# Performance work log

Measured on AMD Instinct MI355X. Metric: run time of the kernel, lower is better.

## Reference

```python
import jax, jax.numpy as jnp
import numpy as np

HEAD_NUM = 16
HIDDEN = 1024
HEAD_DIM = HIDDEN // HEAD_NUM


def setup_inputs() -> dict:
    key = jax.random.key(0)
    ks = jax.random.split(key, 9)
    B, S, D = 1, 4096, HIDDEN
    scale = 1.0 / np.sqrt(D)
    inp = {
        "x": jax.random.normal(ks[0], (B, S, D), jnp.float32),
        "wq": jax.random.normal(ks[1], (D, D), jnp.float32) * scale,
        "bq": jnp.zeros((D,), jnp.float32),
        "wk": jax.random.normal(ks[2], (D, D), jnp.float32) * scale,
        "bk": jnp.zeros((D,), jnp.float32),
        "wv": jax.random.normal(ks[3], (D, D), jnp.float32) * scale,
        "bv": jnp.zeros((D,), jnp.float32),
        "wo": jax.random.normal(ks[4], (D, D), jnp.float32) * scale,
        "bo": jnp.zeros((D,), jnp.float32),
    }
    return inp


def reference(x, wq, bq, wk, bk, wv, bv, wo, bo):
    B, S, D = x.shape
    H, Hd = HEAD_NUM, HEAD_DIM
    # QKV projections (weights stored as [in, out])
    q = (x @ wq + bq).reshape(B, S, H, Hd).transpose(0, 2, 1, 3)  # [B,H,S,Hd]
    k = (x @ wk + bk).reshape(B, S, H, Hd).transpose(0, 2, 1, 3)
    v = (x @ wv + bv).reshape(B, S, H, Hd).transpose(0, 2, 1, 3)
    scores = jnp.einsum("bhqd,bhkd->bhqk", q, k) / jnp.sqrt(jnp.float32(Hd))
    attn = jax.nn.softmax(scores, axis=-1)  # dropout in eval mode = identity
    out = jnp.einsum("bhqk,bhkd->bhqd", attn, v)
    out = out.transpose(0, 2, 1, 3).reshape(B, S, D)
    return out @ wo + bo
```

## Files before the change

### kernel.cpp

```cpp
#include <hip/hip_runtime.h>

#define S_LEN  4096
#define DMODEL 1024
#define NHEAD  16
#define HDIM   64

#define QSCALE 0.18033688011112042f

typedef unsigned short u16;
typedef unsigned int   u32;
typedef __bf16 bf16x8 __attribute__((ext_vector_type(8)));
typedef float  f32x4  __attribute__((ext_vector_type(4)));

static __device__ __forceinline__ u16 f2b(float f) {
    union { __bf16 b; u16 u; } c; c.b = (__bf16)f; return c.u;
}

static __device__ __forceinline__ float fexp2(float x) {
#if __has_builtin(__builtin_amdgcn_exp2f)
    return __builtin_amdgcn_exp2f(x);
#else
    return __expf(x * 0.6931471805599453f);
#endif
}

typedef __attribute__((address_space(3))) u32 lds_u32_t;
typedef __attribute__((address_space(1))) const u32 glb_u32_t;
static __device__ __forceinline__ void gload_lds16(const u16* g, u16* l) {
    __builtin_amdgcn_global_load_lds((glb_u32_t*)g, (lds_u32_t*)l, 16, 0, 0);
}

__global__ __launch_bounds__(256)
void convert_x(const float* __restrict__ x, u16* __restrict__ xb) {
    const int i0 = (blockIdx.x * 256 + threadIdx.x) * 8;
    float4 a = *reinterpret_cast<const float4*>(x + i0);
    float4 b = *reinterpret_cast<const float4*>(x + i0 + 4);
    u16 o[8] = {f2b(a.x), f2b(a.y), f2b(a.z), f2b(a.w),
                f2b(b.x), f2b(b.y), f2b(b.z), f2b(b.w)};
    *reinterpret_cast<uint4*>(xb + i0) = *reinterpret_cast<uint4*>(o);
}

__global__ __launch_bounds__(256)
void transpose_w4(const float* __restrict__ w0, const float* __restrict__ w1,
                  const float* __restrict__ w2, const float* __restrict__ w3,
                  u16* __restrict__ wT) {
    const int z = blockIdx.z;
    const float* w = (z == 0) ? w0 : (z == 1) ? w1 : (z == 2) ? w2 : w3;
    u16* dst0 = wT + (size_t)z * DMODEL * DMODEL;
    const int k0 = blockIdx.x * 64, n0 = blockIdx.y * 64;
    const int t = threadIdx.x;
    __shared__ u16 T[64][72];
    const int kk = t >> 4, nn = (t & 15) * 4;
    #pragma unroll
    for (int i = 0; i < 4; ++i) {
        float4 v = *reinterpret_cast<const float4*>(w + (size_t)(k0 + kk + i * 16) * DMODEL + n0 + nn);
        T[nn + 0][kk + i * 16] = f2b(v.x);
        T[nn + 1][kk + i * 16] = f2b(v.y);
        T[nn + 2][kk + i * 16] = f2b(v.z);
        T[nn + 3][kk + i * 16] = f2b(v.w);
    }
    __syncthreads();
    const int n = t >> 2, kc = (t & 3) * 16;
    uint4 r0 = *reinterpret_cast<const uint4*>(&T[n][kc]);
    uint4 r1 = *reinterpret_cast<const uint4*>(&T[n][kc + 8]);
    u16* dst = dst0 + (size_t)(n0 + n) * DMODEL + k0 + kc;
    *reinterpret_cast<uint4*>(dst)     = r0;
    *reinterpret_cast<uint4*>(dst + 8) = r1;
}

template<int MODE>
__global__ __launch_bounds__(256, 2)
void gemm128(const u16* __restrict__ A, const u16* __restrict__ BT,
             const float* __restrict__ b0, const float* __restrict__ b1,
             const float* __restrict__ b2, void* __restrict__ Cout) {
    const int m0 = blockIdx.x * 128;
    const int ny = blockIdx.y;
    const int tz = (MODE == 0) ? (ny >> 3) : 0;
    const int n0 = (MODE == 0) ? ((ny & 7) * 128) : (ny * 128);
    const int tid = threadIdx.x, lane = tid & 63, w = tid >> 6;
    const int wr = w >> 1, wc = w & 1;
    const int fm = lane & 15, fq = lane >> 4;

    __shared__ u16 As[128][32];
    __shared__ u16 Bs[128][32];

    const u16* Bb = BT + (size_t)tz * DMODEL * DMODEL;

    f32x4 acc[4][4];
    #pragma unroll
    for (int i = 0; i < 4; ++i)
        #pragma unroll
        for (int t = 0; t < 4; ++t) acc[i][t] = f32x4{0.f, 0.f, 0.f, 0.f};

    const int srow = lane >> 2, scol = (lane & 3) * 8;

    for (int k0 = 0; k0 < DMODEL; k0 += 32) {
        #pragma unroll
        for (int r = 0; r < 2; ++r) {
            const int rowA = w * 32 + r * 16;
            gload_lds16(A  + (size_t)(m0 + rowA + srow) * DMODEL + k0 + scol, &As[rowA][0]);
            gload_lds16(Bb + (size_t)(n0 + rowA + srow) * DMODEL + k0 + scol, &Bs[rowA][0]);
        }
        __syncthreads();
        bf16x8 af[4], bf[4];
        #pragma unroll
        for (int i = 0; i < 4; ++i) af[i] = *reinterpret_cast<const bf16x8*>(&As[wr * 64 + i * 16 + fm][fq * 8]);
        #pragma unroll
        for (int t = 0; t < 4; ++t) bf[t] = *reinterpret_cast<const bf16x8*>(&Bs[wc * 64 + t * 16 + fm][fq * 8]);
        #pragma unroll
        for (int i = 0; i < 4; ++i)
            #pragma unroll
            for (int t = 0; t < 4; ++t)
                acc[i][t] = __builtin_amdgcn_mfma_f32_16x16x32_bf16(af[i], bf[t], acc[i][t], 0, 0, 0);
        __syncthreads();
    }

    const float* bp = (MODE == 0) ? ((tz == 0) ? b0 : (tz == 1) ? b1 : b2) : b0;
    const float scl = (MODE == 0 && tz == 0) ? QSCALE : 1.0f;
    #pragma unroll
    for (int t = 0; t < 4; ++t) {
        const int col = n0 + wc * 64 + t * 16 + fm;
        const float bias = bp[col];
        if (MODE == 0 && tz == 2) {
            const int hh = col >> 6, d = col & 63;
            u16* vb = (u16*)Cout + (size_t)2 * S_LEN * DMODEL +
                      ((size_t)hh * HDIM + d) * S_LEN;
            #pragma unroll
            for (int i = 0; i < 4; ++i) {
                const int row0 = m0 + wr * 64 + i * 16 + fq * 4;
                u16 o[4] = {f2b(acc[i][t][0] + bias), f2b(acc[i][t][1] + bias),
                            f2b(acc[i][t][2] + bias), f2b(acc[i][t][3] + bias)};
                *reinterpret_cast<uint2*>(vb + row0) = *reinterpret_cast<uint2*>(o);
            }
        } else {
            #pragma unroll
            for (int i = 0; i < 4; ++i) {
                #pragma unroll
                for (int r = 0; r < 4; ++r) {
                    const int row = m0 + wr * 64 + i * 16 + fq * 4 + r;
                    const float v = (acc[i][t][r] + bias) * scl;
                    if (MODE == 0) {
                        const int hh = col >> 6, d = col & 63;
                        ((u16*)Cout)[(size_t)tz * S_LEN * DMODEL +
                                     ((size_t)hh * S_LEN + row) * HDIM + d] = f2b(v);
                    } else {
                        ((float*)Cout)[(size_t)row * DMODEL + col] = v;
                    }
                }
            }
        }
    }
}

__global__ __launch_bounds__(256, 2)
void gemm_o(const u16* __restrict__ A, const u16* __restrict__ BT,
            const float* __restrict__ bias, float* __restrict__ C) {
    const int m0 = blockIdx.x * 128;
    const int n0 = blockIdx.y * 64;
    const int tid = threadIdx.x, lane = tid & 63, w = tid >> 6;
    const int fm = lane & 15, fq = lane >> 4;

    __shared__ u16 As[128][32];
    __shared__ u16 Bs[64][32];

    f32x4 acc[2][4];
    #pragma unroll
    for (int i = 0; i < 2; ++i)
        #pragma unroll
        for (int t = 0; t < 4; ++t) acc[i][t] = f32x4{0.f, 0.f, 0.f, 0.f};

    const int srow = lane >> 2, scol = (lane & 3) * 8;

    for (int k0 = 0; k0 < DMODEL; k0 += 32) {
        #pragma unroll
        for (int r = 0; r < 2; ++r) {
            const int rowA = w * 32 + r * 16;
            gload_lds16(A + (size_t)(m0 + rowA + srow) * DMODEL + k0 + scol, &As[rowA][0]);
        }
        gload_lds16(BT + (size_t)(n0 + w * 16 + srow) * DMODEL + k0 + scol, &Bs[w * 16][0]);
        __syncthreads();
        bf16x8 af[2], bf[4];
        #pragma unroll
        for (int i = 0; i < 2; ++i) af[i] = *reinterpret_cast<const bf16x8*>(&As[w * 32 + i * 16 + fm][fq * 8]);
        #pragma unroll
        for (int t = 0; t < 4; ++t) bf[t] = *reinterpret_cast<const bf16x8*>(&Bs[t * 16 + fm][fq * 8]);
        #pragma unroll
        for (int i = 0; i < 2; ++i)
            #pragma unroll
            for (int t = 0; t < 4; ++t)
                acc[i][t] = __builtin_amdgcn_mfma_f32_16x16x32_bf16(af[i], bf[t], acc[i][t], 0, 0, 0);
        __syncthreads();
    }

    #pragma unroll
    for (int t = 0; t < 4; ++t) {
        const int col = n0 + t * 16 + fm;
        const float b = bias[col];
        #pragma unroll
        for (int i = 0; i < 2; ++i) {
            #pragma unroll
            for (int r = 0; r < 4; ++r) {
                const int row = m0 + w * 32 + i * 16 + fq * 4 + r;
                C[(size_t)row * DMODEL + col] = acc[i][t][r] + b;
            }
        }
    }
}

template<int NSPLIT>
__global__ __launch_bounds__(256, 4)
void attn_kernel(const u16* __restrict__ Q, const u16* __restrict__ K,
                 const u16* __restrict__ V, void* __restrict__ Optr,
                 float* __restrict__ Lp) {
    const int qt = blockIdx.x, h = blockIdx.y;
    const int sp = (NSPLIT > 1) ? blockIdx.z : 0;
    const int tid = threadIdx.x, lane = tid & 63, wid = tid >> 6;
    const int fm = lane & 15, fq = lane >> 4;

    __shared__ alignas(16) u16 Pt[128][36];
    __shared__ alignas(16) u16 Ks[64][68];
    __shared__ alignas(16) u16 Vt[64][68];

    const u16* Qh = Q + (size_t)h * S_LEN * HDIM;
    const u16* Kh = K + (size_t)h * S_LEN * HDIM;
    const u16* Vh = V + (size_t)h * S_LEN * HDIM;

    const int srow = tid >> 2, sch = (tid & 3) * 16;

    bf16x8 qf[2][2];
    #pragma unroll
    for (int rb = 0; rb < 2; ++rb) {
        const u16* qsrc = Qh + (size_t)(qt * 128 + wid * 32 + rb * 16 + fm) * HDIM + fq * 8;
        qf[rb][0] = *reinterpret_cast<const bf16x8*>(qsrc);
        qf[rb][1] = *reinterpret_cast<const bf16x8*>(qsrc + 32);
    }

    float rsum[2] = {0.f, 0.f};
    f32x4 oacc[2][4];
    #pragma unroll
    for (int rb = 0; rb < 2; ++rb)
        #pragma unroll
        for (int t = 0; t < 4; ++t) oacc[rb][t] = f32x4{0.f, 0.f, 0.f, 0.f};

    const int TOT  = S_LEN / 64;
    const int base = TOT / NSPLIT;
    const int rem  = TOT - base * NSPLIT;
    const int kt0  = sp * base + (sp < rem ? sp : rem);
    const int NT   = base + (sp < rem ? 1 : 0);

    uint4 kr0, kr1, vr0, vr1;
    {
        const u16* ks = Kh + (size_t)(kt0 * 64 + srow) * HDIM + sch;
        kr0 = *reinterpret_cast<const uint4*>(ks);
        kr1 = *reinterpret_cast<const uint4*>(ks + 8);
        const u16* vs = Vh + (size_t)srow * S_LEN + kt0 * 64 + sch;
        vr0 = *reinterpret_cast<const uint4*>(vs);
        vr1 = *reinterpret_cast<const uint4*>(vs + 8);
    }

    for (int it = 0; it < NT; ++it) {
        const int kt = kt0 + it;
        __syncthreads();
        *reinterpret_cast<uint4*>(&Ks[srow][sch])     = kr0;
        *reinterpret_cast<uint4*>(&Ks[srow][sch + 8]) = kr1;
        *reinterpret_cast<uint4*>(&Vt[srow][sch])     = vr0;
        *reinterpret_cast<uint4*>(&Vt[srow][sch + 8]) = vr1;
        __syncthreads();

        if (it + 1 < NT) {
            const u16* ks = Kh + (size_t)((kt + 1) * 64 + srow) * HDIM + sch;
            kr0 = *reinterpret_cast<const uint4*>(ks);
            kr1 = *reinterpret_cast<const uint4*>(ks + 8);
            const u16* vs = Vh + (size_t)srow * S_LEN + (kt + 1) * 64 + sch;
            vr0 = *reinterpret_cast<const uint4*>(vs);
            vr1 = *reinterpret_cast<const uint4*>(vs + 8);
        }

        f32x4 sacc[2][4];
        #pragma unroll
        for (int rb = 0; rb < 2; ++rb)
            #pragma unroll
            for (int mt = 0; mt < 4; ++mt) sacc[rb][mt] = f32x4{0.f, 0.f, 0.f, 0.f};
        __builtin_amdgcn_s_setprio(1);
        #pragma unroll
        for (int kk2 = 0; kk2 < 2; ++kk2) {
            #pragma unroll
            for (int mt = 0; mt < 4; ++mt) {
                bf16x8 kf = *reinterpret_cast<const bf16x8*>(&Ks[mt * 16 + fm][kk2 * 32 + fq * 8]);
                #pragma unroll
                for (int rb = 0; rb < 2; ++rb)
                    sacc[rb][mt] = __builtin_amdgcn_mfma_f32_16x16x32_bf16(kf, qf[rb][kk2], sacc[rb][mt], 0, 0, 0);
            }
        }
        __builtin_amdgcn_s_setprio(0);

        #pragma unroll
        for (int ph = 0; ph < 2; ++ph) {
            #pragma unroll
            for (int rb = 0; rb < 2; ++rb) {
                #pragma unroll
                for (int m2 = 0; m2 < 2; ++m2) {
                    const int mt = ph * 2 + m2;
                    u32 pk[2];
                    float e0 = fexp2(sacc[rb][mt][0]);
                    float e1 = fexp2(sacc[rb][mt][1]);
                    float e2 = fexp2(sacc[rb][mt][2]);
                    float e3 = fexp2(sacc[rb][mt][3]);
                    rsum[rb] += (e0 + e1) + (e2 + e3);
                    pk[0] = (u32)f2b(e0) | ((u32)f2b(e1) << 16);
                    pk[1] = (u32)f2b(e2) | ((u32)f2b(e3) << 16);
                    *reinterpret_cast<uint2*>(&Pt[wid * 32 + rb * 16 + fm][m2 * 16 + fq * 4]) =
                        uint2{pk[0], pk[1]};
                }
            }
            bf16x8 af[2];
            #pragma unroll
            for (int rb = 0; rb < 2; ++rb)
                af[rb] = *reinterpret_cast<const bf16x8*>(&Pt[wid * 32 + rb * 16 + fm][fq * 8]);
            __builtin_amdgcn_s_setprio(1);
            #pragma unroll
            for (int t = 0; t < 4; ++t) {
                bf16x8 bf = *reinterpret_cast<const bf16x8*>(&Vt[t * 16 + fm][ph * 32 + fq * 8]);
                #pragma unroll
                for (int rb = 0; rb < 2; ++rb)
                    oacc[rb][t] = __builtin_amdgcn_mfma_f32_16x16x32_bf16(af[rb], bf, oacc[rb][t], 0, 0, 0);
            }
            __builtin_amdgcn_s_setprio(0);
        }
    }

    if (NSPLIT > 1) {
        float* Op = (float*)Optr + (size_t)sp * S_LEN * DMODEL;
        #pragma unroll
        for (int rb = 0; rb < 2; ++rb) {
            float rs = rsum[rb];
            rs += __shfl_xor(rs, 16, 64);
            rs += __shfl_xor(rs, 32, 64);
            if (fq == 0)
                Lp[(size_t)sp * NHEAD * S_LEN + (size_t)h * S_LEN +
                   qt * 128 + wid * 32 + rb * 16 + fm] = rs;
            #pragma unroll
            for (int t = 0; t < 4; ++t) {
                const int d = t * 16 + fm;
                #pragma unroll
                for (int r = 0; r < 4; ++r) {
                    const int row = qt * 128 + wid * 32 + rb * 16 + fq * 4 + r;
                    Op[(size_t)row * DMODEL + h * HDIM + d] = oacc[rb][t][r];
                }
            }
        }
    } else {
        float l[2][4];
        #pragma unroll
        for (int rb = 0; rb < 2; ++rb) {
            float rs = rsum[rb];
            rs += __shfl_xor(rs, 16, 64);
            rs += __shfl_xor(rs, 32, 64);
            #pragma unroll
            for (int r = 0; r < 4; ++r) l[rb][r] = __shfl(rs, fq * 4 + r, 64);
        }
        u16* O = (u16*)Optr;
        #pragma unroll
        for (int rb = 0; rb < 2; ++rb)
            #pragma unroll
            for (int t = 0; t < 4; ++t) {
                const int d = t * 16 + fm;
                #pragma unroll
                for (int r = 0; r < 4; ++r) {
                    const int row = qt * 128 + wid * 32 + rb * 16 + fq * 4 + r;
                    O[(size_t)row * DMODEL + h * HDIM + d] = f2b(oacc[rb][t][r] / l[rb][r]);
                }
            }
    }
}

template<int NS>
__global__ __launch_bounds__(256)
void combine_o(const float* __restrict__ Op, const float* __restrict__ Lp,
               u16* __restrict__ Ob) {
    const size_t i = ((size_t)blockIdx.x * 256 + threadIdx.x) * 4;
    const int row = (int)(i >> 10), col = (int)(i & 1023);
    const int h = col >> 6;
    float ax = 0.f, ay = 0.f, az = 0.f, aw = 0.f, l = 0.f;
    #pragma unroll
    for (int s = 0; s < NS; ++s) {
        float4 v = *reinterpret_cast<const float4*>(Op + (size_t)s * S_LEN * DMODEL + i);
        ax += v.x; ay += v.y; az += v.z; aw += v.w;
        l += Lp[(size_t)s * NHEAD * S_LEN + (size_t)h * S_LEN + row];
    }
    const float inv = 1.0f / l;
    u16 o[4] = {f2b(ax * inv), f2b(ay * inv), f2b(az * inv), f2b(aw * inv)};
    *reinterpret_cast<uint2*>(Ob + i) = *reinterpret_cast<uint2*>(o);
}

extern "C" void kernel_launch(void* const* d_in, const int* in_sizes, int n_in,
                              void* d_out, int out_size, void* d_ws, size_t ws_size,
                              hipStream_t stream) {
    const float* x  = (const float*)d_in[0];
    const float* wq = (const float*)d_in[1];
    const float* bq = (const float*)d_in[2];
    const float* wk = (const float*)d_in[3];
    const float* bk = (const float*)d_in[4];
    const float* wv = (const float*)d_in[5];
    const float* bv = (const float*)d_in[6];
    const float* wo = (const float*)d_in[7];
    const float* bo = (const float*)d_in[8];

    u16* ws = (u16*)d_ws;
    const size_t MW  = (size_t)DMODEL * DMODEL;
    const size_t NX  = (size_t)S_LEN * DMODEL;
    const size_t TSZ = (size_t)NHEAD * S_LEN * HDIM;

    u16* xb = ws;
    u16* WT = xb + NX;
    u16* Qb = WT + 4 * MW;
    u16* Ob = Qb + 3 * TSZ;
    float* Op = (float*)(Ob + NX);
    float* Lp2 = Op + (size_t)2 * NX;
    const size_t need2 = (size_t)((char*)(Lp2 + (size_t)2 * NHEAD * S_LEN) - (char*)d_ws);

    hipLaunchKernelGGL(convert_x, dim3(NX / 2048), dim3(256), 0, stream, x, xb);
    hipLaunchKernelGGL(transpose_w4, dim3(16, 16, 4), dim3(256), 0, stream, wq, wk, wv, wo, WT);

    hipLaunchKernelGGL((gemm128<0>), dim3(S_LEN / 128, 24), dim3(256), 0, stream,
                       xb, WT, bq, bk, bv, (void*)Qb);

    if (ws_size >= need2) {
        hipLaunchKernelGGL((attn_kernel<2>), dim3(S_LEN / 128, NHEAD, 2), dim3(256), 0, stream,
                           Qb, Qb + TSZ, Qb + 2 * TSZ, (void*)Op, Lp2);
        hipLaunchKernelGGL((combine_o<2>), dim3((S_LEN * DMODEL / 4) / 256), dim3(256), 0, stream,
                           Op, Lp2, Ob);
    } else {
        hipLaunchKernelGGL((attn_kernel<1>), dim3(S_LEN / 128, NHEAD, 1), dim3(256), 0, stream,
                           Qb, Qb + TSZ, Qb + 2 * TSZ, (void*)Ob, (float*)nullptr);
    }

    hipLaunchKernelGGL(gemm_o, dim3(S_LEN / 128, DMODEL / 64), dim3(256), 0, stream,
                       Ob, WT + 3 * MW, bo, (float*)d_out);
}
```

Baseline: 245.0 us.

## Swap MFMA operands for vectorized Q/K/O epilogue stores and remap attention blocks per XCD

For the Q and K projections and the output projection, the MFMA operands are swapped so each lane holds four consecutive output columns. This lets the epilogues write packed 8-byte bf16 or 16-byte float4 stores instead of scattered scalar stores, and load the bias as a float4. The split attention kernel moves to a 1D grid whose block index is decoded so each head is pinned to one XCD, aiming for better L2 reuse of K/V. The uneven-split remainder logic is dropped, which assumes the key-tile count divides evenly by the split.

Result: slower. 258.0 us (+5.3%).

```diff
diff --git a/kernel.cpp b/kernel.cpp
--- a/kernel.cpp
+++ b/kernel.cpp
@@ -68,18 +68,18 @@
     *reinterpret_cast<uint4*>(dst + 8) = r1;
 }
 
-template<int MODE>
 __global__ __launch_bounds__(256, 2)
-void gemm128(const u16* __restrict__ A, const u16* __restrict__ BT,
-             const float* __restrict__ b0, const float* __restrict__ b1,
-             const float* __restrict__ b2, void* __restrict__ Cout) {
+void gemm_qkv(const u16* __restrict__ A, const u16* __restrict__ BT,
+              const float* __restrict__ b0, const float* __restrict__ b1,
+              const float* __restrict__ b2, u16* __restrict__ Cout) {
     const int m0 = blockIdx.x * 128;
     const int ny = blockIdx.y;
-    const int tz = (MODE == 0) ? (ny >> 3) : 0;
-    const int n0 = (MODE == 0) ? ((ny & 7) * 128) : (ny * 128);
+    const int tz = ny >> 3;
+    const int n0 = (ny & 7) * 128;
     const int tid = threadIdx.x, lane = tid & 63, w = tid >> 6;
     const int wr = w >> 1, wc = w & 1;
     const int fm = lane & 15, fq = lane >> 4;
+    const bool ct = (tz < 2);
 
     __shared__ u16 As[128][32];
     __shared__ u16 Bs[128][32];
@@ -107,46 +107,55 @@
         for (int i = 0; i < 4; ++i) af[i] = *reinterpret_cast<const bf16x8*>(&As[wr * 64 + i * 16 + fm][fq * 8]);
         #pragma unroll
         for (int t = 0; t < 4; ++t) bf[t] = *reinterpret_cast<const bf16x8*>(&Bs[wc * 64 + t * 16 + fm][fq * 8]);
-        #pragma unroll
-        for (int i = 0; i < 4; ++i)
-            #pragma unroll
-            for (int t = 0; t < 4; ++t)
-                acc[i][t] = __builtin_amdgcn_mfma_f32_16x16x32_bf16(af[i], bf[t], acc[i][t], 0, 0, 0);
-        __syncthreads();
-    }
-
-    const float* bp = (MODE == 0) ? ((tz == 0) ? b0 : (tz == 1) ? b1 : b2) : b0;
-    const float scl = (MODE == 0 && tz == 0) ? QSCALE : 1.0f;
-    #pragma unroll
-    for (int t = 0; t < 4; ++t) {
-        const int col = n0 + wc * 64 + t * 16 + fm;
-        const float bias = bp[col];
-        if (MODE == 0 && tz == 2) {
+        if (ct) {
+            #pragma unroll
+            for (int i = 0; i < 4; ++i)
+                #pragma unroll
+                for (int t = 0; t < 4; ++t)
+                    acc[i][t] = __builtin_amdgcn_mfma_f32_16x16x32_bf16(bf[t], af[i], acc[i][t], 0, 0, 0);
+        } else {
+            #pragma unroll
+            for (int i = 0; i < 4; ++i)
+                #pragma unroll
+                for (int t = 0; t < 4; ++t)
+                    acc[i][t] = __builtin_amdgcn_mfma_f32_16x16x32_bf16(af[i], bf[t], acc[i][t], 0, 0, 0);
+        }
+        __syncthreads();
+    }
+
+    const float* bp = (tz == 0) ? b0 : (tz == 1) ? b1 : b2;
+    u16* base = Cout + (size_t)tz * S_LEN * DMODEL;
+    if (ct) {
+        const float scl = (tz == 0) ? QSCALE : 1.0f;
+        #pragma unroll
+        for (int t = 0; t < 4; ++t) {
+            const int nb = n0 + wc * 64 + t * 16 + fq * 4;
+            const int hh = nb >> 6, d0 = nb & 63;
+            const float4 b4 = *reinterpret_cast<const float4*>(bp + nb);
+            #pragma unroll
+            for (int i = 0; i < 4; ++i) {
+                const int m = m0 + wr * 64 + i * 16 + fm;
+                u16 o[4] = {f2b((acc[i][t][0] + b4.x) * scl),
+                            f2b((acc[i][t][1] + b4.y) * scl),
+                            f2b((acc[i][t][2] + b4.z) * scl),
+                            f2b((acc[i][t][3] + b4.w) * scl)};
+                *reinterpret_cast<uint2*>(base + ((size_t)hh * S_LEN + m) * HDIM + d0) =
+                    *reinterpret_cast<uint2*>(o);
+            }
+        }
+    } else {
+        #pragma unroll
+        for (int t = 0; t < 4; ++t) {
+            const int col = n0 + wc * 64 + t * 16 + fm;
             const int hh = col >> 6, d = col & 63;
-            u16* vb = (u16*)Cout + (size_t)2 * S_LEN * DMODEL +
-                      ((size_t)hh * HDIM + d) * S_LEN;
+            const float bias = bp[col];
+            u16* vb = base + ((size_t)hh * HDIM + d) * S_LEN;
             #pragma unroll
             for (int i = 0; i < 4; ++i) {
                 const int row0 = m0 + wr * 64 + i * 16 + fq * 4;
                 u16 o[4] = {f2b(acc[i][t][0] + bias), f2b(acc[i][t][1] + bias),
                             f2b(acc[i][t][2] + bias), f2b(acc[i][t][3] + bias)};
                 *reinterpret_cast<uint2*>(vb + row0) = *reinterpret_cast<uint2*>(o);
-            }
-        } else {
-            #pragma unroll
-            for (int i = 0; i < 4; ++i) {
-                #pragma unroll
-                for (int r = 0; r < 4; ++r) {
-                    const int row = m0 + wr * 64 + i * 16 + fq * 4 + r;
-                    const float v = (acc[i][t][r] + bias) * scl;
-                    if (MODE == 0) {
-                        const int hh = col >> 6, d = col & 63;
-                        ((u16*)Cout)[(size_t)tz * S_LEN * DMODEL +
-                                     ((size_t)hh * S_LEN + row) * HDIM + d] = f2b(v);
-                    } else {
-                        ((float*)Cout)[(size_t)row * DMODEL + col] = v;
-                    }
-                }
             }
         }
     }
@@ -188,21 +197,20 @@
         for (int i = 0; i < 2; ++i)
             #pragma unroll
             for (int t = 0; t < 4; ++t)
-                acc[i][t] = __builtin_amdgcn_mfma_f32_16x16x32_bf16(af[i], bf[t], acc[i][t], 0, 0, 0);
+                acc[i][t] = __builtin_amdgcn_mfma_f32_16x16x32_bf16(bf[t], af[i], acc[i][t], 0, 0, 0);
         __syncthreads();
     }
 
     #pragma unroll
     for (int t = 0; t < 4; ++t) {
-        const int col = n0 + t * 16 + fm;
-        const float b = bias[col];
+        const int nb = n0 + t * 16 + fq * 4;
+        const float4 b4 = *reinterpret_cast<const float4*>(bias + nb);
         #pragma unroll
         for (int i = 0; i < 2; ++i) {
-            #pragma unroll
-            for (int r = 0; r < 4; ++r) {
-                const int row = m0 + w * 32 + i * 16 + fq * 4 + r;
-                C[(size_t)row * DMODEL + col] = acc[i][t][r] + b;
-            }
+            const int m = m0 + w * 32 + i * 16 + fm;
+            float4 o = {acc[i][t][0] + b4.x, acc[i][t][1] + b4.y,
+                        acc[i][t][2] + b4.z, acc[i][t][3] + b4.w};
+            *reinterpret_cast<float4*>(C + (size_t)m * DMODEL + nb) = o;
         }
     }
 }
@@ -212,8 +220,18 @@
 void attn_kernel(const u16* __restrict__ Q, const u16* __restrict__ K,
                  const u16* __restrict__ V, void* __restrict__ Optr,
                  float* __restrict__ Lp) {
-    const int qt = blockIdx.x, h = blockIdx.y;
-    const int sp = (NSPLIT > 1) ? blockIdx.z : 0;
+    int qt, h, sp;
+    if (NSPLIT > 1) {
+        const int bid = blockIdx.x;
+        const int xcd = bid & 7;
+        const int g = bid >> 3;
+        qt = g & 31;
+        const int hs = g >> 5;
+        h = xcd | ((hs & 1) << 3);
+        sp = hs >> 1;
+    } else {
+        qt = blockIdx.x; h = blockIdx.y; sp = 0;
+    }
     const int tid = threadIdx.x, lane = tid & 63, wid = tid >> 6;
     const int fm = lane & 15, fq = lane >> 4;
 
@@ -243,10 +261,8 @@
         for (int t = 0; t < 4; ++t) oacc[rb][t] = f32x4{0.f, 0.f, 0.f, 0.f};
 
     const int TOT  = S_LEN / 64;
-    const int base = TOT / NSPLIT;
-    const int rem  = TOT - base * NSPLIT;
-    const int kt0  = sp * base + (sp < rem ? sp : rem);
-    const int NT   = base + (sp < rem ? 1 : 0);
+    const int NT   = TOT / NSPLIT;
+    const int kt0  = sp * NT;
 
     uint4 kr0, kr1, vr0, vr1;
     {
@@ -422,16 +438,16 @@
     hipLaunchKernelGGL(convert_x, dim3(NX / 2048), dim3(256), 0, stream, x, xb);
     hipLaunchKernelGGL(transpose_w4, dim3(16, 16, 4), dim3(256), 0, stream, wq, wk, wv, wo, WT);
 
-    hipLaunchKernelGGL((gemm128<0>), dim3(S_LEN / 128, 24), dim3(256), 0, stream,
-                       xb, WT, bq, bk, bv, (void*)Qb);
+    hipLaunchKernelGGL(gemm_qkv, dim3(S_LEN / 128, 24), dim3(256), 0, stream,
+                       xb, WT, bq, bk, bv, Qb);
 
     if (ws_size >= need2) {
-        hipLaunchKernelGGL((attn_kernel<2>), dim3(S_LEN / 128, NHEAD, 2), dim3(256), 0, stream,
+        hipLaunchKernelGGL((attn_kernel<2>), dim3(1024), dim3(256), 0, stream,
                            Qb, Qb + TSZ, Qb + 2 * TSZ, (void*)Op, Lp2);
         hipLaunchKernelGGL((combine_o<2>), dim3((S_LEN * DMODEL / 4) / 256), dim3(256), 0, stream,
                            Op, Lp2, Ob);
     } else {
-        hipLaunchKernelGGL((attn_kernel<1>), dim3(S_LEN / 128, NHEAD, 1), dim3(256), 0, stream,
+        hipLaunchKernelGGL((attn_kernel<1>), dim3(S_LEN / 128, NHEAD), dim3(256), 0, stream,
                            Qb, Qb + TSZ, Qb + 2 * TSZ, (void*)Ob, (float*)nullptr);
     }
 
```
